# Performance work log

Hardware: AMD Instinct MI355X
Metric: run time of the kernel (lower is better)

Reference implementation:

```python
import jax, jax.numpy as jnp
import numpy as np

B, S, H, NH = 1, 2048, 4096, 32
HD = H // NH
INV_NORM = 1.0 / np.sqrt(HD)


def _alibi_slopes(n_heads):
    # standard Bloom ALiBi slopes
    closest_pow2 = 2 ** int(np.floor(np.log2(n_heads)))
    base = 2.0 ** (-(2.0 ** -(np.log2(closest_pow2) - 3)))
    slopes = base ** np.arange(1, closest_pow2 + 1)
    if closest_pow2 != n_heads:
        extra_base = 2.0 ** (-(2.0 ** -(np.log2(2 * closest_pow2) - 3)))
        extra = extra_base ** np.arange(1, 2 * (n_heads - closest_pow2) + 1, 2)
        slopes = np.concatenate([slopes, extra])
    return slopes.astype(np.float32)


def setup_inputs() -> dict:
    key = jax.random.key(0)
    ks = jax.random.split(key, 6)
    hidden_states = jax.random.normal(ks[0], (B, S, H), dtype=jnp.float32)
    residual = jax.random.normal(ks[1], (B, S, H), dtype=jnp.float32)
    # ALiBi bias: slopes[h] * position, shape [B*NH, 1, S]
    slopes = jnp.asarray(_alibi_slopes(NH))  # [NH]
    pos = jnp.arange(S, dtype=jnp.float32)  # [S]
    alibi = (slopes[:, None] * pos[None, :])[:, None, :]  # [NH,1,S]
    alibi = jnp.tile(alibi, (B, 1, 1))  # [B*NH,1,S]
    # causal mask: True = masked out
    attention_mask = ~jnp.tril(jnp.ones((S, S), dtype=bool))[None, None]  # [1,1,S,S]
    qkv_w = jax.random.normal(ks[2], (3 * H, H), dtype=jnp.float32) * 0.02
    qkv_b = jax.random.normal(ks[3], (3 * H,), dtype=jnp.float32) * 0.02
    dense_w = jax.random.normal(ks[4], (H, H), dtype=jnp.float32) * 0.02
    dense_b = jax.random.normal(ks[5], (H,), dtype=jnp.float32) * 0.02
    return {
        "hidden_states": hidden_states,
        "residual": residual,
        "alibi": alibi,
        "attention_mask": attention_mask,
        "qkv_w": qkv_w,
        "qkv_b": qkv_b,
        "dense_w": dense_w,
        "dense_b": dense_b,
    }


def reference(hidden_states, residual, alibi, attention_mask, qkv_w, qkv_b, dense_w, dense_b):
    b, s, h = hidden_states.shape
    fused = hidden_states @ qkv_w.T + qkv_b  # [B,S,3H]
    fused = fused.reshape(b, s, NH, 3, HD)  # per-head interleaved q,k,v
    q, k, v = fused[..., 0, :], fused[..., 1, :], fused[..., 2, :]  # [B,S,NH,HD]
    # scores = beta*alibi + inv_norm * q @ k^T
    scores = jnp.einsum("bqnd,bknd->bnqk", q, k) * INV_NORM
    scores = scores + alibi.reshape(b, NH, 1, s)  # broadcast over q
    scores = jnp.where(attention_mask, jnp.finfo(scores.dtype).min, scores)
    probs = jax.nn.softmax(scores.astype(jnp.float32), axis=-1)  # [B,NH,S,S]
    ctx = jnp.einsum("bnqk,bknd->bqnd", probs, v).reshape(b, s, h)
    out = ctx @ dense_w.T + dense_b
    return residual + out  # dropout_add with p=0 / eval mode
```

## Files before the change

kernel.cpp:

```cpp
#include <hip/hip_runtime.h>
#include <cstdint>
#include <cstddef>

typedef unsigned short u16;
typedef __attribute__((ext_vector_type(8))) __bf16 bf16x8;
typedef __attribute__((ext_vector_type(4))) float f32x4;

#define S_LEN   2048
#define H_DIM   4096
#define NH_N    32
#define HD_N    128
#define QK_LD   8192

__device__ __forceinline__ u16 f2b(float f) {
  union { float f; unsigned u; } v; v.f = f;
  unsigned r = v.u + 0x7fffu + ((v.u >> 16) & 1u);
  return (u16)(r >> 16);
}

__device__ __forceinline__ void gl2lds16(const void* g, void* l) {
  __builtin_amdgcn_global_load_lds((__attribute__((address_space(1))) void*)g,
                                   (__attribute__((address_space(3))) void*)l,
                                   16, 0, 0);
}

__global__ __launch_bounds__(256) void cvt_kernel(const float* __restrict__ src,
                                                  u16* __restrict__ dst, int n8) {
  int i = blockIdx.x * 256 + threadIdx.x;
  if (i >= n8) return;
  const float4* s4 = (const float4*)src;
  float4 a = s4[i * 2], b = s4[i * 2 + 1];
  union { u16 o[8]; uint4 v; } u;
  u.o[0] = f2b(a.x); u.o[1] = f2b(a.y); u.o[2] = f2b(a.z); u.o[3] = f2b(a.w);
  u.o[4] = f2b(b.x); u.o[5] = f2b(b.y); u.o[6] = f2b(b.z); u.o[7] = f2b(b.w);
  ((uint4*)dst)[i] = u.v;
}

template <int OUTF32>
__global__ __launch_bounds__(256, 2)
void gemm_kernel(const u16* __restrict__ A, const u16* __restrict__ B,
                 const float* __restrict__ bias, const float* __restrict__ resid,
                 u16* __restrict__ outQK, u16* __restrict__ outVT,
                 float* __restrict__ outF,
                 int M, int N, int K) {
  __shared__ __align__(16) u16 As[128 * 64];
  __shared__ __align__(16) u16 Bs[128 * 64];
  const int tid  = threadIdx.x;
  const int lane = tid & 63;
  const int wave = tid >> 6;
  const int l15  = lane & 15;
  const int quad = lane >> 4;
  const int m0 = blockIdx.y * 128;
  const int n0 = blockIdx.x * 128;
  const int wm = (wave & 1) * 64;
  const int wn = (wave >> 1) * 64;

  f32x4 acc[4][4] = {};

  int sRow[4], sCol[4];
#pragma unroll
  for (int it = 0; it < 4; ++it) {
    int slot = wave * 256 + it * 64 + lane;
    int row  = slot >> 3;
    int kc   = (slot & 7) ^ (row & 7);
    sRow[it] = row;
    sCol[it] = kc * 8;
  }
  const u16* Ag = A + (size_t)m0 * K;
  const u16* Bg = B + (size_t)n0 * K;

  for (int kb = 0; kb < K; kb += 64) {
#pragma unroll
    for (int it = 0; it < 4; ++it) {
      int base = (wave * 256 + it * 64) * 8;
      gl2lds16(Ag + (size_t)sRow[it] * K + kb + sCol[it], &As[base]);
      gl2lds16(Bg + (size_t)sRow[it] * K + kb + sCol[it], &Bs[base]);
    }
    __syncthreads();
#pragma unroll
    for (int s = 0; s < 2; ++s) {
      const int kc = s * 4 + quad;
      bf16x8 af[4], bfr[4];
#pragma unroll
      for (int i = 0; i < 4; ++i) {
        int ra = wm + i * 16 + l15;
        af[i]  = *(const bf16x8*)&As[(ra * 8 + (kc ^ (ra & 7))) * 8];
        int rb = wn + i * 16 + l15;
        bfr[i] = *(const bf16x8*)&Bs[(rb * 8 + (kc ^ (rb & 7))) * 8];
      }
#pragma unroll
      for (int i = 0; i < 4; ++i)
#pragma unroll
        for (int j = 0; j < 4; ++j)
          acc[i][j] = __builtin_amdgcn_mfma_f32_16x16x32_bf16(af[i], bfr[j], acc[i][j], 0, 0, 0);
    }
    __syncthreads();
  }

#pragma unroll
  for (int i = 0; i < 4; ++i) {
    int rowb = m0 + wm + i * 16 + quad * 4;
#pragma unroll
    for (int j = 0; j < 4; ++j) {
      int c0 = n0 + wn + j * 16;
      float bb = bias[c0 + l15];
      if (OUTF32) {
#pragma unroll
        for (int r = 0; r < 4; ++r) {
          size_t rowoff = (size_t)(rowb + r) * N;
          outF[rowoff + c0 + l15] = acc[i][j][r] + bb + resid[rowoff + c0 + l15];
        }
      } else {
        int head = c0 / 384;
        int rem  = c0 % 384;
        int part = rem >> 7;
        if (part == 2) {
          int d = (rem & 127) + l15;
          union { ushort4 v; u16 e[4]; } pk;
#pragma unroll
          for (int r = 0; r < 4; ++r) pk.e[r] = f2b(acc[i][j][r] + bb);
          *(ushort4*)&outVT[(size_t)head * (HD_N * S_LEN) + (size_t)d * S_LEN + rowb] = pk.v;
        } else {
          int colq = head * 256 + part * 128 + (rem & 127) + l15;
#pragma unroll
          for (int r = 0; r < 4; ++r)
            outQK[(size_t)(rowb + r) * QK_LD + colq] = f2b(acc[i][j][r] + bb);
        }
      }
    }
  }
}

__global__ __launch_bounds__(256, 2)
void attn_kernel(const u16* __restrict__ QK, const u16* __restrict__ VT,
                 const float* __restrict__ alibi, u16* __restrict__ CTX) {
  __shared__ __align__(16) u16 Ks[2][64 * 128];
  __shared__ __align__(16) u16 Vs[2][128 * 64];
  __shared__ __align__(16) u16 Ps[4 * 1024];
  const int tid  = threadIdx.x;
  const int lane = tid & 63;
  const int wave = tid >> 6;
  const int l15  = lane & 15;
  const int quad = lane >> 4;
  const int qt   = (int)gridDim.x - 1 - (int)blockIdx.x;
  const int head = blockIdx.y;
  const int q0   = qt * 64;
  const float c1 = 0.08838834764831845f * 1.4426950408889634f;
  const float slope2 = alibi[head * S_LEN + 1] * 1.4426950408889634f;

  const u16* Kbase = QK + head * 256 + 128;
  const u16* Vbase = VT + (size_t)head * (HD_N * S_LEN);

  int kRow[4], kCol[4], vRow[4], vCol[4];
#pragma unroll
  for (int it = 0; it < 4; ++it) {
    int slot = wave * 256 + it * 64 + lane;
    int kr = slot >> 4;
    kRow[it] = kr;
    kCol[it] = ((slot & 15) ^ (kr & 15)) * 8;
    int d = slot >> 3;
    vRow[it] = d;
    vCol[it] = ((slot & 7) ^ (d & 7)) * 8;
  }

  bf16x8 qf[4];
  {
    const u16* qp = QK + (size_t)(q0 + wave * 16 + l15) * QK_LD + head * 256;
#pragma unroll
    for (int s = 0; s < 4; ++s) qf[s] = *(const bf16x8*)(qp + s * 32 + quad * 8);
  }

  float m_i[4], l_i[4];
#pragma unroll
  for (int r = 0; r < 4; ++r) { m_i[r] = -3.0e38f; l_i[r] = 0.0f; }
  f32x4 acc[8] = {};

  const int nk = qt + 1;

#pragma unroll
  for (int it = 0; it < 4; ++it) {
    int base = (wave * 256 + it * 64) * 8;
    gl2lds16(Kbase + (size_t)kRow[it] * QK_LD + kCol[it], &Ks[0][base]);
    gl2lds16(Vbase + (size_t)vRow[it] * S_LEN + vCol[it], &Vs[0][base]);
  }
  __syncthreads();

  int cur = 0;
  for (int kt = 0; kt < nk; ++kt) {
    const int k0 = kt * 64;
    if (kt + 1 < nk) {
      const int kn = k0 + 64;
#pragma unroll
      for (int it = 0; it < 4; ++it) {
        int base = (wave * 256 + it * 64) * 8;
        gl2lds16(Kbase + (size_t)(kn + kRow[it]) * QK_LD + kCol[it], &Ks[cur ^ 1][base]);
        gl2lds16(Vbase + (size_t)vRow[it] * S_LEN + kn + vCol[it], &Vs[cur ^ 1][base]);
      }
    }

    f32x4 sc[4] = {};
#pragma unroll
    for (int s = 0; s < 4; ++s) {
      const int kc = s * 4 + quad;
      bf16x8 kf[4];
#pragma unroll
      for (int j = 0; j < 4; ++j) {
        int row = j * 16 + l15;
        kf[j] = *(const bf16x8*)&Ks[cur][(row * 16 + (kc ^ (row & 15))) * 8];
      }
#pragma unroll
      for (int j = 0; j < 4; ++j)
        sc[j] = __builtin_amdgcn_mfma_f32_16x16x32_bf16(qf[s], kf[j], sc[j], 0, 0, 0);
    }

    const bool diag = (kt == qt);
    float xv[4][4];
    float mt[4] = { -3.0e38f, -3.0e38f, -3.0e38f, -3.0e38f };
#pragma unroll
    for (int j = 0; j < 4; ++j) {
      int key  = k0 + j * 16 + l15;
      float al = slope2 * (float)key;
#pragma unroll
      for (int r = 0; r < 4; ++r) {
        float x = sc[j][r] * c1 + al;
        if (diag) {
          int qrow = q0 + wave * 16 + quad * 4 + r;
          if (key > qrow) x = -3.0e38f;
        }
        xv[j][r] = x;
        mt[r] = fmaxf(mt[r], x);
      }
    }
#pragma unroll
    for (int r = 0; r < 4; ++r) {
      float v = mt[r];
      v = fmaxf(v, __shfl_xor(v, 1));
      v = fmaxf(v, __shfl_xor(v, 2));
      v = fmaxf(v, __shfl_xor(v, 4));
      v = fmaxf(v, __shfl_xor(v, 8));
      mt[r] = fmaxf(m_i[r], v);
    }
    float alpha[4], psum[4];
#pragma unroll
    for (int r = 0; r < 4; ++r) {
      alpha[r] = exp2f(m_i[r] - mt[r]);
      m_i[r] = mt[r];
      psum[r] = 0.0f;
    }
#pragma unroll
    for (int j = 0; j < 4; ++j) {
      int col = j * 16 + l15;
      int kc  = col >> 3;
#pragma unroll
      for (int r = 0; r < 4; ++r) {
        float p = exp2f(xv[j][r] - m_i[r]);
        psum[r] += p;
        int qrow = quad * 4 + r;
        Ps[wave * 1024 + (qrow * 8 + (kc ^ (qrow & 7))) * 8 + (col & 7)] = f2b(p);
      }
    }
#pragma unroll
    for (int r = 0; r < 4; ++r) {
      float v = psum[r];
      v += __shfl_xor(v, 1);
      v += __shfl_xor(v, 2);
      v += __shfl_xor(v, 4);
      v += __shfl_xor(v, 8);
      l_i[r] = l_i[r] * alpha[r] + v;
    }
#pragma unroll
    for (int t = 0; t < 8; ++t)
#pragma unroll
      for (int r = 0; r < 4; ++r) acc[t][r] *= alpha[r];

#pragma unroll
    for (int s = 0; s < 2; ++s) {
      const int kc = s * 4 + quad;
      bf16x8 pf = *(const bf16x8*)&Ps[wave * 1024 + (l15 * 8 + (kc ^ (l15 & 7))) * 8];
#pragma unroll
      for (int t = 0; t < 8; ++t) {
        int row = t * 16 + l15;
        bf16x8 vf = *(const bf16x8*)&Vs[cur][(row * 8 + (kc ^ (row & 7))) * 8];
        acc[t] = __builtin_amdgcn_mfma_f32_16x16x32_bf16(pf, vf, acc[t], 0, 0, 0);
      }
    }
    __syncthreads();
    cur ^= 1;
  }

#pragma unroll
  for (int r = 0; r < 4; ++r) {
    float inv = 1.0f / l_i[r];
    size_t rowoff = (size_t)(q0 + wave * 16 + quad * 4 + r) * H_DIM;
#pragma unroll
    for (int t = 0; t < 8; ++t)
      CTX[rowoff + head * HD_N + t * 16 + l15] = f2b(acc[t][r] * inv);
  }
}

extern "C" void kernel_launch(void* const* d_in, const int* in_sizes, int n_in,
                              void* d_out, int out_size, void* d_ws, size_t ws_size,
                              hipStream_t stream) {
  const float* hidden   = (const float*)d_in[0];
  const float* residual = (const float*)d_in[1];
  const float* alibi    = (const float*)d_in[2];
  const float* qkv_w    = (const float*)d_in[4];
  const float* qkv_b    = (const float*)d_in[5];
  const float* dense_w  = (const float*)d_in[6];
  const float* dense_b  = (const float*)d_in[7];
  float* out = (float*)d_out;

  u16* Xb  = (u16*)d_ws;
  u16* Wq  = Xb + (size_t)S_LEN * H_DIM;
  u16* Wd  = Wq + (size_t)3 * H_DIM * H_DIM;
  u16* QKb = Wd + (size_t)H_DIM * H_DIM;
  u16* VT  = QKb + (size_t)S_LEN * QK_LD;
  u16* CTX = VT + (size_t)NH_N * HD_N * S_LEN;

  {
    int n8 = S_LEN * H_DIM / 8;
    cvt_kernel<<<dim3((n8 + 255) / 256), 256, 0, stream>>>(hidden, Xb, n8);
  }
  {
    int n8 = 3 * H_DIM * H_DIM / 8;
    cvt_kernel<<<dim3((n8 + 255) / 256), 256, 0, stream>>>(qkv_w, Wq, n8);
  }
  {
    int n8 = H_DIM * H_DIM / 8;
    cvt_kernel<<<dim3((n8 + 255) / 256), 256, 0, stream>>>(dense_w, Wd, n8);
  }

  gemm_kernel<0><<<dim3(3 * H_DIM / 128, S_LEN / 128), 256, 0, stream>>>(
      Xb, Wq, qkv_b, nullptr, QKb, VT, nullptr, S_LEN, 3 * H_DIM, H_DIM);

  attn_kernel<<<dim3(S_LEN / 64, NH_N), 256, 0, stream>>>(QKb, VT, alibi, CTX);

  gemm_kernel<1><<<dim3(H_DIM / 128, S_LEN / 128), 256, 0, stream>>>(
      CTX, Wd, dense_b, residual, nullptr, nullptr, out, S_LEN, H_DIM, H_DIM);
}
```

Before: 835.0 us.

## Widen attention query tile to 128 rows and merge conversion kernels

The attention kernel now runs 512-thread blocks covering 128 query rows, so each K/V tile loaded into LDS is shared by eight waves instead of four. The grid becomes a 1D launch that pairs long and short causal query tiles per head, and the MFMA sections are raised in wave priority with s_setprio. The three fp32-to-bf16 conversion launches are merged into one kernel, which also switches to one float4 per thread. The larger block uses more LDS and registers, which may lower occupancy.

After: 775.9 us. -7.1%, faster.

```diff
diff --git a/kernel.cpp b/kernel.cpp
--- a/kernel.cpp
+++ b/kernel.cpp
@@ -24,16 +24,22 @@
                                    16, 0, 0);
 }
 
-__global__ __launch_bounds__(256) void cvt_kernel(const float* __restrict__ src,
-                                                  u16* __restrict__ dst, int n8) {
-  int i = blockIdx.x * 256 + threadIdx.x;
-  if (i >= n8) return;
-  const float4* s4 = (const float4*)src;
-  float4 a = s4[i * 2], b = s4[i * 2 + 1];
-  union { u16 o[8]; uint4 v; } u;
+__global__ __launch_bounds__(256)
+void cvt3_kernel(const float* __restrict__ s0, u16* __restrict__ d0, int n0,
+                 const float* __restrict__ s1, u16* __restrict__ d1, int n1,
+                 const float* __restrict__ s2, u16* __restrict__ d2, int n2,
+                 int b0, int b1) {
+  int blk = blockIdx.x;
+  const float* src; u16* dst; int n; int base;
+  if (blk < b0)      { src = s0; dst = d0; n = n0; base = blk; }
+  else if (blk < b1) { src = s1; dst = d1; n = n1; base = blk - b0; }
+  else               { src = s2; dst = d2; n = n2; base = blk - b1; }
+  int i = base * 256 + threadIdx.x;
+  if (i >= n) return;
+  float4 a = ((const float4*)src)[i];
+  union { u16 o[4]; ushort4 v; } u;
   u.o[0] = f2b(a.x); u.o[1] = f2b(a.y); u.o[2] = f2b(a.z); u.o[3] = f2b(a.w);
-  u.o[4] = f2b(b.x); u.o[5] = f2b(b.y); u.o[6] = f2b(b.z); u.o[7] = f2b(b.w);
-  ((uint4*)dst)[i] = u.v;
+  ((ushort4*)dst)[i] = u.v;
 }
 
 template <int OUTF32>
@@ -131,36 +137,41 @@
   }
 }
 
-__global__ __launch_bounds__(256, 2)
+__global__ __launch_bounds__(512, 4)
 void attn_kernel(const u16* __restrict__ QK, const u16* __restrict__ VT,
                  const float* __restrict__ alibi, u16* __restrict__ CTX) {
   __shared__ __align__(16) u16 Ks[2][64 * 128];
   __shared__ __align__(16) u16 Vs[2][128 * 64];
-  __shared__ __align__(16) u16 Ps[4 * 1024];
+  __shared__ __align__(16) u16 Ps[8 * 1024];
   const int tid  = threadIdx.x;
   const int lane = tid & 63;
   const int wave = tid >> 6;
   const int l15  = lane & 15;
   const int quad = lane >> 4;
-  const int qt   = (int)gridDim.x - 1 - (int)blockIdx.x;
-  const int head = blockIdx.y;
-  const int q0   = qt * 64;
+  const int lin  = blockIdx.x;
+  const int ub   = lin & 255;
+  const int vb   = lin >> 8;
+  const int head = ub & 31;
+  const int idx  = ub >> 5;
+  const int qt   = vb ? idx : (15 - idx);
+  const int q0   = qt * 128;
   const float c1 = 0.08838834764831845f * 1.4426950408889634f;
   const float slope2 = alibi[head * S_LEN + 1] * 1.4426950408889634f;
 
   const u16* Kbase = QK + head * 256 + 128;
   const u16* Vbase = VT + (size_t)head * (HD_N * S_LEN);
 
-  int kRow[4], kCol[4], vRow[4], vCol[4];
-#pragma unroll
-  for (int it = 0; it < 4; ++it) {
-    int slot = wave * 256 + it * 64 + lane;
+  int kRow[2], kCol[2], vRow[2], vCol[2], sBase[2];
+#pragma unroll
+  for (int it = 0; it < 2; ++it) {
+    int slot = it * 512 + tid;
     int kr = slot >> 4;
     kRow[it] = kr;
     kCol[it] = ((slot & 15) ^ (kr & 15)) * 8;
     int d = slot >> 3;
     vRow[it] = d;
     vCol[it] = ((slot & 7) ^ (d & 7)) * 8;
+    sBase[it] = (it * 512 + wave * 64) * 8;
   }
 
   bf16x8 qf[4];
@@ -175,13 +186,12 @@
   for (int r = 0; r < 4; ++r) { m_i[r] = -3.0e38f; l_i[r] = 0.0f; }
   f32x4 acc[8] = {};
 
-  const int nk = qt + 1;
-
-#pragma unroll
-  for (int it = 0; it < 4; ++it) {
-    int base = (wave * 256 + it * 64) * 8;
-    gl2lds16(Kbase + (size_t)kRow[it] * QK_LD + kCol[it], &Ks[0][base]);
-    gl2lds16(Vbase + (size_t)vRow[it] * S_LEN + vCol[it], &Vs[0][base]);
+  const int nk = 2 * qt + 2;
+
+#pragma unroll
+  for (int it = 0; it < 2; ++it) {
+    gl2lds16(Kbase + (size_t)kRow[it] * QK_LD + kCol[it], &Ks[0][sBase[it]]);
+    gl2lds16(Vbase + (size_t)vRow[it] * S_LEN + vCol[it], &Vs[0][sBase[it]]);
   }
   __syncthreads();
 
@@ -191,14 +201,14 @@
     if (kt + 1 < nk) {
       const int kn = k0 + 64;
 #pragma unroll
-      for (int it = 0; it < 4; ++it) {
-        int base = (wave * 256 + it * 64) * 8;
-        gl2lds16(Kbase + (size_t)(kn + kRow[it]) * QK_LD + kCol[it], &Ks[cur ^ 1][base]);
-        gl2lds16(Vbase + (size_t)vRow[it] * S_LEN + kn + vCol[it], &Vs[cur ^ 1][base]);
+      for (int it = 0; it < 2; ++it) {
+        gl2lds16(Kbase + (size_t)(kn + kRow[it]) * QK_LD + kCol[it], &Ks[cur ^ 1][sBase[it]]);
+        gl2lds16(Vbase + (size_t)vRow[it] * S_LEN + kn + vCol[it], &Vs[cur ^ 1][sBase[it]]);
       }
     }
 
     f32x4 sc[4] = {};
+    __builtin_amdgcn_s_setprio(1);
 #pragma unroll
     for (int s = 0; s < 4; ++s) {
       const int kc = s * 4 + quad;
@@ -212,8 +222,9 @@
       for (int j = 0; j < 4; ++j)
         sc[j] = __builtin_amdgcn_mfma_f32_16x16x32_bf16(qf[s], kf[j], sc[j], 0, 0, 0);
     }
-
-    const bool diag = (kt == qt);
+    __builtin_amdgcn_s_setprio(0);
+
+    const bool maskT = (kt >= 2 * qt);
     float xv[4][4];
     float mt[4] = { -3.0e38f, -3.0e38f, -3.0e38f, -3.0e38f };
 #pragma unroll
@@ -223,7 +234,7 @@
 #pragma unroll
       for (int r = 0; r < 4; ++r) {
         float x = sc[j][r] * c1 + al;
-        if (diag) {
+        if (maskT) {
           int qrow = q0 + wave * 16 + quad * 4 + r;
           if (key > qrow) x = -3.0e38f;
         }
@@ -273,6 +284,7 @@
 #pragma unroll
       for (int r = 0; r < 4; ++r) acc[t][r] *= alpha[r];
 
+    __builtin_amdgcn_s_setprio(1);
 #pragma unroll
     for (int s = 0; s < 2; ++s) {
       const int kc = s * 4 + quad;
@@ -284,6 +296,7 @@
         acc[t] = __builtin_amdgcn_mfma_f32_16x16x32_bf16(pf, vf, acc[t], 0, 0, 0);
       }
     }
+    __builtin_amdgcn_s_setprio(0);
     __syncthreads();
     cur ^= 1;
   }
@@ -318,22 +331,18 @@
   u16* CTX = VT + (size_t)NH_N * HD_N * S_LEN;
 
   {
-    int n8 = S_LEN * H_DIM / 8;
-    cvt_kernel<<<dim3((n8 + 255) / 256), 256, 0, stream>>>(hidden, Xb, n8);
-  }
-  {
-    int n8 = 3 * H_DIM * H_DIM / 8;
-    cvt_kernel<<<dim3((n8 + 255) / 256), 256, 0, stream>>>(qkv_w, Wq, n8);
-  }
-  {
-    int n8 = H_DIM * H_DIM / 8;
-    cvt_kernel<<<dim3((n8 + 255) / 256), 256, 0, stream>>>(dense_w, Wd, n8);
+    int n0 = S_LEN * H_DIM / 4;
+    int n1 = 3 * H_DIM * H_DIM / 4;
+    int n2 = H_DIM * H_DIM / 4;
+    int nb0 = (n0 + 255) / 256, nb1 = (n1 + 255) / 256, nb2 = (n2 + 255) / 256;
+    cvt3_kernel<<<dim3(nb0 + nb1 + nb2), 256, 0, stream>>>(
+        hidden, Xb, n0, qkv_w, Wq, n1, dense_w, Wd, n2, nb0, nb0 + nb1);
   }
 
   gemm_kernel<0><<<dim3(3 * H_DIM / 128, S_LEN / 128), 256, 0, stream>>>(
       Xb, Wq, qkv_b, nullptr, QKb, VT, nullptr, S_LEN, 3 * H_DIM, H_DIM);
 
-  attn_kernel<<<dim3(S_LEN / 64, NH_N), 256, 0, stream>>>(QKb, VT, alibi, CTX);
+  attn_kernel<<<dim3(512), 512, 0, stream>>>(QKb, VT, alibi, CTX);
 
   gemm_kernel<1><<<dim3(H_DIM / 128, S_LEN / 128), 256, 0, stream>>>(
       CTX, Wd, dense_b, residual, nullptr, nullptr, out, S_LEN, H_DIM, H_DIM);
```
